# Optimization experiments

Hardware: AMD Instinct MI355X
Metric: run time of the kernel (lower is better)

The kernel has to match this reference:

```python
import jax, jax.numpy as jnp
import numpy as np


def setup_inputs() -> dict:
    key = jax.random.key(0)
    B, C, H, W = 64, 128, 64, 64
    x = jax.random.normal(key, (B, C, H, W), dtype=jnp.float32)
    return {"x": x}


def reference(x) -> jnp.ndarray:
    # Covariance pooling: y = x_flat @ I_hat @ x_flat^T with
    # I_hat = (1/M) I - (1/M^2) ones(M,M).
    # Algebraically identical to (1/M) * (x - mean)(x - mean)^T, which
    # avoids materializing the MxM centering matrix.
    B, C, H, W = x.shape
    M = H * W
    xf = x.reshape(B, C, M)
    xc = xf - jnp.mean(xf, axis=2, keepdims=True)  # center over spatial dim
    y = jnp.einsum('bcm,bdm->bcd', xc, xc) / M     # [B, C, C]
    return y
```

## Files before the change

kernel.cpp:

```cpp
#include <hip/hip_runtime.h>

typedef __bf16 bf16x8 __attribute__((ext_vector_type(8)));
typedef float  f32x4  __attribute__((ext_vector_type(4)));
typedef unsigned short us8 __attribute__((ext_vector_type(8)));

#define B_      64
#define C_      128
#define M_      4096
#define KCHUNK  8
#define KC      (M_ / KCHUNK)
#define BK      64
#define NSLAB   (KC / BK)
#define LSTR    72

__device__ __forceinline__ unsigned short f2bf(float f) {
  unsigned u = __builtin_bit_cast(unsigned, f);
  u += 0x7fffu + ((u >> 16) & 1u);
  return (unsigned short)(u >> 16);
}
__device__ __forceinline__ float bf2f(unsigned short h) {
  unsigned u = ((unsigned)h) << 16;
  return __builtin_bit_cast(float, u);
}

__global__ __launch_bounds__(512, 4) void covpool_main(
    const float* __restrict__ x, unsigned short* __restrict__ Gp, float* __restrict__ Sp) {
  __shared__ unsigned short As[2][C_ * LSTR];

  const int tid  = threadIdx.x;
  const int b    = blockIdx.x >> 3;
  const int ch   = blockIdx.x & 7;

  const int row  = tid >> 3;
  const int col8 = tid & 7;

  const float* xp0 = x + ((size_t)(b * C_ + row) * M_) + (size_t)ch * KC + col8 * 8;
  const float* xp1 = xp0 + (size_t)64 * M_;

  const int lane = tid & 63;
  const int wave = tid >> 6;
  const int row0 = (wave >> 2) << 6;
  const int col0 = (wave & 3) << 5;
  const int lrow = lane & 15;
  const int quad = lane >> 4;

  f32x4 acc[4][2];
#pragma unroll
  for (int i = 0; i < 4; ++i)
#pragma unroll
    for (int j = 0; j < 2; ++j)
      acc[i][j] = (f32x4){0.f, 0.f, 0.f, 0.f};

  float sum0 = 0.f, sum1 = 0.f;

  float4 a0, a1, a2, a3, b0, b1, b2, b3;

  a0 = ((const float4*)xp0)[0]; a1 = ((const float4*)xp0)[1];
  a2 = ((const float4*)xp1)[0]; a3 = ((const float4*)xp1)[1];

#define STAGE(BUF, R0, R1, R2, R3)                                                  \
  {                                                                                 \
    sum0 += (R0.x + R0.y) + (R0.z + R0.w) + (R1.x + R1.y) + (R1.z + R1.w);          \
    sum1 += (R2.x + R2.y) + (R2.z + R2.w) + (R3.x + R3.y) + (R3.z + R3.w);          \
    us8 v0 = { f2bf(R0.x), f2bf(R0.y), f2bf(R0.z), f2bf(R0.w),                      \
               f2bf(R1.x), f2bf(R1.y), f2bf(R1.z), f2bf(R1.w) };                    \
    us8 v1 = { f2bf(R2.x), f2bf(R2.y), f2bf(R2.z), f2bf(R2.w),                      \
               f2bf(R3.x), f2bf(R3.y), f2bf(R3.z), f2bf(R3.w) };                    \
    *(__shared__ us8*)&As[BUF][row * LSTR + col8 * 8]        = v0;                  \
    *(__shared__ us8*)&As[BUF][(64 + row) * LSTR + col8 * 8] = v1;                  \
  }

#define COMPUTE(BUF)                                                                \
  {                                                                                 \
    _Pragma("unroll")                                                               \
    for (int ks = 0; ks < 2; ++ks) {                                                \
      const int koff = ks * 32 + quad * 8;                                          \
      bf16x8 af[4], bfr[2];                                                         \
      _Pragma("unroll")                                                             \
      for (int i = 0; i < 4; ++i)                                                   \
        af[i] = *(const __shared__ bf16x8*)&As[BUF][(row0 + i * 16 + lrow) * LSTR + koff]; \
      _Pragma("unroll")                                                             \
      for (int j = 0; j < 2; ++j)                                                   \
        bfr[j] = *(const __shared__ bf16x8*)&As[BUF][(col0 + j * 16 + lrow) * LSTR + koff]; \
      _Pragma("unroll")                                                             \
      for (int i = 0; i < 4; ++i)                                                   \
        _Pragma("unroll")                                                           \
        for (int j = 0; j < 2; ++j)                                                 \
          acc[i][j] = __builtin_amdgcn_mfma_f32_16x16x32_bf16(af[i], bfr[j], acc[i][j], 0, 0, 0); \
    }                                                                               \
  }

#pragma unroll
  for (int s = 0; s < NSLAB; s += 2) {
    {
      const float* p0 = xp0 + (size_t)(s + 1) * BK;
      const float* p1 = xp1 + (size_t)(s + 1) * BK;
      b0 = ((const float4*)p0)[0]; b1 = ((const float4*)p0)[1];
      b2 = ((const float4*)p1)[0]; b3 = ((const float4*)p1)[1];
    }
    STAGE(0, a0, a1, a2, a3);
    __syncthreads();
    COMPUTE(0);
    if (s + 2 < NSLAB) {
      const float* p0 = xp0 + (size_t)(s + 2) * BK;
      const float* p1 = xp1 + (size_t)(s + 2) * BK;
      a0 = ((const float4*)p0)[0]; a1 = ((const float4*)p0)[1];
      a2 = ((const float4*)p1)[0]; a3 = ((const float4*)p1)[1];
    }
    STAGE(1, b0, b1, b2, b3);
    __syncthreads();
    COMPUTE(1);
  }

  unsigned short* gout = Gp + (((size_t)ch * B_ + b) << 14);
#pragma unroll
  for (int i = 0; i < 4; ++i)
#pragma unroll
    for (int j = 0; j < 2; ++j)
#pragma unroll
      for (int rr = 0; rr < 4; ++rr)
        gout[(size_t)(row0 + i * 16 + quad * 4 + rr) * C_ + (col0 + j * 16 + lrow)] =
            f2bf(acc[i][j][rr]);

  sum0 += __shfl_xor(sum0, 1); sum0 += __shfl_xor(sum0, 2); sum0 += __shfl_xor(sum0, 4);
  sum1 += __shfl_xor(sum1, 1); sum1 += __shfl_xor(sum1, 2); sum1 += __shfl_xor(sum1, 4);
  if ((tid & 7) == 0) {
    float* sout = Sp + (((size_t)ch * B_ + b) << 7);
    sout[row]      = sum0;
    sout[64 + row] = sum1;
  }
}

__global__ __launch_bounds__(256) void covpool_fix(
    const unsigned short* __restrict__ Gp, const float* __restrict__ Sp,
    float* __restrict__ y) {
  const int idx = (blockIdx.x * 256 + threadIdx.x) * 4;
  const int bb  = idx >> 14;
  const int rem = idx & 16383;
  const int cc  = rem >> 7;
  const int dd  = rem & 127;
  float g0 = 0.f, g1 = 0.f, g2 = 0.f, g3 = 0.f, sc = 0.f;
  float4 sd = {0.f, 0.f, 0.f, 0.f};
#pragma unroll
  for (int ch = 0; ch < KCHUNK; ++ch) {
    ushort4 gv = *(const ushort4*)&Gp[(((size_t)ch * B_ + bb) << 14) + rem];
    g0 += bf2f(gv.x); g1 += bf2f(gv.y); g2 += bf2f(gv.z); g3 += bf2f(gv.w);
    const float* sp = Sp + (((size_t)ch * B_ + bb) << 7);
    sc += sp[cc];
    float4 s4 = *(const float4*)&sp[dd];
    sd.x += s4.x; sd.y += s4.y; sd.z += s4.z; sd.w += s4.w;
  }
  const float invM = 1.f / (float)M_;
  const float scm = sc * invM;
  float4 out = { g0 * invM - scm * (sd.x * invM), g1 * invM - scm * (sd.y * invM),
                 g2 * invM - scm * (sd.z * invM), g3 * invM - scm * (sd.w * invM) };
  *(float4*)&y[idx] = out;
}

extern "C" void kernel_launch(void* const* d_in, const int* in_sizes, int n_in,
                              void* d_out, int out_size, void* d_ws, size_t ws_size,
                              hipStream_t stream) {
  const float* x = (const float*)d_in[0];
  float* out = (float*)d_out;
  unsigned short* wsG = (unsigned short*)d_ws;
  float* wsS = (float*)(wsG + (size_t)KCHUNK * B_ * C_ * C_);
  covpool_main<<<dim3(B_ * KCHUNK), dim3(512), 0, stream>>>(x, wsG, wsS);
  covpool_fix<<<dim3((B_ * C_ * C_) / 1024), dim3(256), 0, stream>>>(wsG, wsS, out);
}
```

Measured before the change: 196.6 us.

## Use native bf16 conversion, reorder prefetch after barrier, widen fix kernel to 8 elements

The bf16 staging now uses the compiler's native float-to-bf16 conversion instead of manual bit rounding, which may map to hardware conversion instructions. The main loop issues the next slab's global loads after the barrier and before the MFMA compute, changing how load latency overlaps with compute and staging. The reduction kernel now processes 8 outputs per thread with 16-byte loads and half as many blocks, to cut instruction count and raise per-thread memory parallelism. The reorder can shift register pressure and change how much load latency stays hidden.

```diff
diff --git a/kernel.cpp b/kernel.cpp
--- a/kernel.cpp
+++ b/kernel.cpp
@@ -2,7 +2,6 @@
 
 typedef __bf16 bf16x8 __attribute__((ext_vector_type(8)));
 typedef float  f32x4  __attribute__((ext_vector_type(4)));
-typedef unsigned short us8 __attribute__((ext_vector_type(8)));
 
 #define B_      64
 #define C_      128
@@ -18,10 +17,8 @@
   u += 0x7fffu + ((u >> 16) & 1u);
   return (unsigned short)(u >> 16);
 }
-__device__ __forceinline__ float bf2f(unsigned short h) {
-  unsigned u = ((unsigned)h) << 16;
-  return __builtin_bit_cast(float, u);
-}
+__device__ __forceinline__ float bf_lo(unsigned u) { return __builtin_bit_cast(float, u << 16); }
+__device__ __forceinline__ float bf_hi(unsigned u) { return __builtin_bit_cast(float, u & 0xffff0000u); }
 
 __global__ __launch_bounds__(512, 4) void covpool_main(
     const float* __restrict__ x, unsigned short* __restrict__ Gp, float* __restrict__ Sp) {
@@ -58,16 +55,16 @@
   a0 = ((const float4*)xp0)[0]; a1 = ((const float4*)xp0)[1];
   a2 = ((const float4*)xp1)[0]; a3 = ((const float4*)xp1)[1];
 
-#define STAGE(BUF, R0, R1, R2, R3)                                                  \
-  {                                                                                 \
-    sum0 += (R0.x + R0.y) + (R0.z + R0.w) + (R1.x + R1.y) + (R1.z + R1.w);          \
-    sum1 += (R2.x + R2.y) + (R2.z + R2.w) + (R3.x + R3.y) + (R3.z + R3.w);          \
-    us8 v0 = { f2bf(R0.x), f2bf(R0.y), f2bf(R0.z), f2bf(R0.w),                      \
-               f2bf(R1.x), f2bf(R1.y), f2bf(R1.z), f2bf(R1.w) };                    \
-    us8 v1 = { f2bf(R2.x), f2bf(R2.y), f2bf(R2.z), f2bf(R2.w),                      \
-               f2bf(R3.x), f2bf(R3.y), f2bf(R3.z), f2bf(R3.w) };                    \
-    *(__shared__ us8*)&As[BUF][row * LSTR + col8 * 8]        = v0;                  \
-    *(__shared__ us8*)&As[BUF][(64 + row) * LSTR + col8 * 8] = v1;                  \
+#define STAGE(BUF, R0, R1, R2, R3)                                                 \
+  {                                                                                \
+    sum0 += (R0.x + R0.y) + (R0.z + R0.w) + (R1.x + R1.y) + (R1.z + R1.w);         \
+    sum1 += (R2.x + R2.y) + (R2.z + R2.w) + (R3.x + R3.y) + (R3.z + R3.w);         \
+    bf16x8 v0 = { (__bf16)R0.x, (__bf16)R0.y, (__bf16)R0.z, (__bf16)R0.w,          \
+                  (__bf16)R1.x, (__bf16)R1.y, (__bf16)R1.z, (__bf16)R1.w };        \
+    bf16x8 v1 = { (__bf16)R2.x, (__bf16)R2.y, (__bf16)R2.z, (__bf16)R2.w,          \
+                  (__bf16)R3.x, (__bf16)R3.y, (__bf16)R3.z, (__bf16)R3.w };        \
+    *(__shared__ bf16x8*)&As[BUF][row * LSTR + col8 * 8]        = v0;              \
+    *(__shared__ bf16x8*)&As[BUF][(64 + row) * LSTR + col8 * 8] = v1;              \
   }
 
 #define COMPUTE(BUF)                                                                \
@@ -92,23 +89,23 @@
 
 #pragma unroll
   for (int s = 0; s < NSLAB; s += 2) {
+    STAGE(0, a0, a1, a2, a3);
+    __syncthreads();
     {
       const float* p0 = xp0 + (size_t)(s + 1) * BK;
       const float* p1 = xp1 + (size_t)(s + 1) * BK;
       b0 = ((const float4*)p0)[0]; b1 = ((const float4*)p0)[1];
       b2 = ((const float4*)p1)[0]; b3 = ((const float4*)p1)[1];
     }
-    STAGE(0, a0, a1, a2, a3);
+    COMPUTE(0);
+    STAGE(1, b0, b1, b2, b3);
     __syncthreads();
-    COMPUTE(0);
     if (s + 2 < NSLAB) {
       const float* p0 = xp0 + (size_t)(s + 2) * BK;
       const float* p1 = xp1 + (size_t)(s + 2) * BK;
       a0 = ((const float4*)p0)[0]; a1 = ((const float4*)p0)[1];
       a2 = ((const float4*)p1)[0]; a3 = ((const float4*)p1)[1];
     }
-    STAGE(1, b0, b1, b2, b3);
-    __syncthreads();
     COMPUTE(1);
   }
 
@@ -134,27 +131,37 @@
 __global__ __launch_bounds__(256) void covpool_fix(
     const unsigned short* __restrict__ Gp, const float* __restrict__ Sp,
     float* __restrict__ y) {
-  const int idx = (blockIdx.x * 256 + threadIdx.x) * 4;
+  const int idx = (blockIdx.x * 256 + threadIdx.x) * 8;
   const int bb  = idx >> 14;
   const int rem = idx & 16383;
   const int cc  = rem >> 7;
   const int dd  = rem & 127;
-  float g0 = 0.f, g1 = 0.f, g2 = 0.f, g3 = 0.f, sc = 0.f;
-  float4 sd = {0.f, 0.f, 0.f, 0.f};
+  float g0 = 0.f, g1 = 0.f, g2 = 0.f, g3 = 0.f;
+  float g4 = 0.f, g5 = 0.f, g6 = 0.f, g7 = 0.f;
+  float sc = 0.f;
+  float4 sd0 = {0.f, 0.f, 0.f, 0.f}, sd1 = {0.f, 0.f, 0.f, 0.f};
 #pragma unroll
   for (int ch = 0; ch < KCHUNK; ++ch) {
-    ushort4 gv = *(const ushort4*)&Gp[(((size_t)ch * B_ + bb) << 14) + rem];
-    g0 += bf2f(gv.x); g1 += bf2f(gv.y); g2 += bf2f(gv.z); g3 += bf2f(gv.w);
+    uint4 gv = *(const uint4*)&Gp[(((size_t)ch * B_ + bb) << 14) + rem];
+    g0 += bf_lo(gv.x); g1 += bf_hi(gv.x);
+    g2 += bf_lo(gv.y); g3 += bf_hi(gv.y);
+    g4 += bf_lo(gv.z); g5 += bf_hi(gv.z);
+    g6 += bf_lo(gv.w); g7 += bf_hi(gv.w);
     const float* sp = Sp + (((size_t)ch * B_ + bb) << 7);
     sc += sp[cc];
-    float4 s4 = *(const float4*)&sp[dd];
-    sd.x += s4.x; sd.y += s4.y; sd.z += s4.z; sd.w += s4.w;
+    float4 s0 = *(const float4*)&sp[dd];
+    float4 s1 = *(const float4*)&sp[dd + 4];
+    sd0.x += s0.x; sd0.y += s0.y; sd0.z += s0.z; sd0.w += s0.w;
+    sd1.x += s1.x; sd1.y += s1.y; sd1.z += s1.z; sd1.w += s1.w;
   }
   const float invM = 1.f / (float)M_;
   const float scm = sc * invM;
-  float4 out = { g0 * invM - scm * (sd.x * invM), g1 * invM - scm * (sd.y * invM),
-                 g2 * invM - scm * (sd.z * invM), g3 * invM - scm * (sd.w * invM) };
-  *(float4*)&y[idx] = out;
+  float4 o0 = { g0 * invM - scm * (sd0.x * invM), g1 * invM - scm * (sd0.y * invM),
+                g2 * invM - scm * (sd0.z * invM), g3 * invM - scm * (sd0.w * invM) };
+  float4 o1 = { g4 * invM - scm * (sd1.x * invM), g5 * invM - scm * (sd1.y * invM),
+                g6 * invM - scm * (sd1.z * invM), g7 * invM - scm * (sd1.w * invM) };
+  *(float4*)&y[idx]     = o0;
+  *(float4*)&y[idx + 4] = o1;
 }
 
 extern "C" void kernel_launch(void* const* d_in, const int* in_sizes, int n_in,
@@ -165,5 +172,5 @@
   unsigned short* wsG = (unsigned short*)d_ws;
   float* wsS = (float*)(wsG + (size_t)KCHUNK * B_ * C_ * C_);
   covpool_main<<<dim3(B_ * KCHUNK), dim3(512), 0, stream>>>(x, wsG, wsS);
-  covpool_fix<<<dim3((B_ * C_ * C_) / 1024), dim3(256), 0, stream>>>(wsG, wsS, out);
+  covpool_fix<<<dim3((B_ * C_ * C_) / 2048), dim3(256), 0, stream>>>(wsG, wsS, out);
 }
```

New measurement: 199.0 us. Within noise of the previous version (+1.2%).
